# Performance work log

Hardware: AMD Instinct MI355X
Metric: run time of the kernel (lower is better)

The kernel has to match this reference:

```python
import jax, jax.numpy as jnp
import numpy as np

INPUT_DIM = 512
HIDDEN_DIM = 512


def _linear_params(key, in_dim, out_dim):
    kw, kb = jax.random.split(key)
    bound = 1.0 / np.sqrt(in_dim)
    W = jax.random.uniform(kw, (out_dim, in_dim), minval=-bound, maxval=bound, dtype=jnp.float32)
    b = jax.random.uniform(kb, (out_dim,), minval=-bound, maxval=bound, dtype=jnp.float32)
    return W, b


def setup_inputs() -> dict:
    key = jax.random.key(0)
    keys = jax.random.split(key, 11)
    B = 8192
    inp = {
        "x_t": jax.random.normal(keys[0], (B, INPUT_DIM), dtype=jnp.float32),
        "h_tm1": jax.random.normal(keys[1], (B, HIDDEN_DIM), dtype=jnp.float32),
        "c_tm1": jax.random.normal(keys[2], (B, HIDDEN_DIM), dtype=jnp.float32),
    }
    names = ["f_x", "f_h", "i_x", "i_h", "g_x", "g_h", "o_x", "o_h"]
    for n, k in zip(names, keys[3:]):
        in_dim = INPUT_DIM if n.endswith("_x") else HIDDEN_DIM
        W, b = _linear_params(k, in_dim, HIDDEN_DIM)
        inp[f"W_{n}"] = W
        inp[f"b_{n}"] = b
    return inp


def reference(x_t, h_tm1, c_tm1,
              W_f_x, b_f_x, W_f_h, b_f_h,
              W_i_x, b_i_x, W_i_h, b_i_h,
              W_g_x, b_g_x, W_g_h, b_g_h,
              W_o_x, b_o_x, W_o_h, b_o_h):
    # Stacked weights: [4, H, D] -> einsum over D gives [B, 4, H].
    Wx = jnp.stack([W_f_x, W_g_x, W_i_x, W_o_x])  # [4, H, Din]
    bx = jnp.stack([b_f_x, b_g_x, b_i_x, b_o_x])  # [4, H]
    Wh = jnp.stack([W_f_h, W_g_h, W_i_h, W_o_h])
    bh = jnp.stack([b_f_h, b_g_h, b_i_h, b_o_h])
    pre = (jnp.einsum('bd,ghd->bgh', x_t, Wx) + bx
           + jnp.einsum('bd,ghd->bgh', h_tm1, Wh) + bh)  # [B, 4, H]
    f_t = jax.nn.sigmoid(pre[:, 0])
    g_t = jnp.tanh(pre[:, 1])
    i_t = jax.nn.sigmoid(pre[:, 2])
    o_t = jax.nn.sigmoid(pre[:, 3])
    c_t = f_t * c_tm1 + i_t * g_t
    h_t = o_t * jnp.tanh(c_t)
    return (h_t, c_t)
```

## Files before the change

### kernel.cpp

```cpp
#include <hip/hip_runtime.h>
#include <cstdint>
#include <cstddef>


typedef __attribute__((ext_vector_type(8))) short short8;
typedef __attribute__((ext_vector_type(4))) float floatx4;

#define AS1(p) ((const __attribute__((address_space(1))) void*)(p))
#define AS3(p) ((__attribute__((address_space(3))) void*)(p))

__device__ __forceinline__ unsigned short f2bf(float f) {
  union { float f; unsigned u; } v; v.f = f;
  unsigned u = v.u;
  return (unsigned short)((u + 0x7fffu + ((u >> 16) & 1u)) >> 16);
}

__global__ void pack_a_kernel(const float* __restrict__ x,
                              const float* __restrict__ h,
                              unsigned short* __restrict__ A) {
  int e4 = blockIdx.x * 256 + threadIdx.x;
  int e = e4 * 4;
  int b = e >> 10;
  int k = e & 1023;
  const float* src = (k < 512) ? (x + b * 512 + k) : (h + b * 512 + (k - 512));
  float4 v = *(const float4*)src;
  ushort4 o;
  o.x = f2bf(v.x); o.y = f2bf(v.y); o.z = f2bf(v.z); o.w = f2bf(v.w);
  *(ushort4*)(A + e) = o;
}

struct WPtrs {
  const float* wx[4]; const float* wh[4];
  const float* bx[4]; const float* bh[4];
};

__global__ void pack_w_kernel(WPtrs P, unsigned short* __restrict__ B,
                              float* __restrict__ bias) {
  int e4 = blockIdx.x * 256 + threadIdx.x;
  int e = e4 * 4;
  int n = e >> 10;
  int k = e & 1023;
  int g = n >> 9, hh = n & 511;
  const float* src = (k < 512) ? (P.wx[g] + hh * 512 + k)
                               : (P.wh[g] + hh * 512 + (k - 512));
  float4 v = *(const float4*)src;
  ushort4 o;
  o.x = f2bf(v.x); o.y = f2bf(v.y); o.z = f2bf(v.z); o.w = f2bf(v.w);
  *(ushort4*)(B + e) = o;
  if (k == 0) bias[n] = P.bx[g][hh] + P.bh[g][hh];
}

__global__ __launch_bounds__(256)
void lstm_gemm_kernel(const unsigned short* __restrict__ A,
                      const unsigned short* __restrict__ B,
                      const float* __restrict__ bias,
                      const float* __restrict__ c_prev,
                      float* __restrict__ h_out,
                      float* __restrict__ c_out) {
  __shared__ __align__(16) char smem[33792];
  __shared__ float biasS[128];

  const int tid  = threadIdx.x;
  const int lane = tid & 63;
  const int w    = tid >> 6;
  const int quad = lane >> 4;
  const int colA = lane & 15;
  const int m0   = blockIdx.x * 128;
  const int h0   = blockIdx.y * 32;

  if (tid < 128) {
    int g = tid >> 5, hh = tid & 31;
    biasS[tid] = bias[g * 512 + h0 + hh];
  }

  const int srow = tid >> 3;
  const int cl   = tid & 7;
  const int cg   = cl ^ (srow & 7);

  floatx4 acc[4][4];
#pragma unroll
  for (int i = 0; i < 4; ++i)
#pragma unroll
    for (int j = 0; j < 4; ++j) acc[i][j] = (floatx4){0.f, 0.f, 0.f, 0.f};

  const int wm = (w >> 1) * 64;
  const int wn = (w & 1) * 64;

  const char* Ag = (const char*)A;
  const char* Bg = (const char*)B;

  for (int kt = 0; kt < 16; ++kt) {
    __syncthreads();
    const int kb = kt * 128;
#pragma unroll
    for (int j = 0; j < 4; ++j) {
      int r = j * 32 + srow;
      __builtin_amdgcn_global_load_lds(
          AS1(Ag + (size_t)(m0 + r) * 2048 + kb + cg * 16),
          AS3(smem + r * 128 + cl * 16), 16, 0, 0);
      __builtin_amdgcn_global_load_lds(
          AS1(Bg + (size_t)(j * 512 + h0 + srow) * 2048 + kb + cg * 16),
          AS3(smem + 16384 + r * 128 + cl * 16), 16, 0, 0);
    }
    __syncthreads();

#pragma unroll
    for (int kk = 0; kk < 2; ++kk) {
      const int off = ((kk * 4 + quad) ^ (lane & 7)) * 16;
      short8 af[4], bfr[4];
#pragma unroll
      for (int mi = 0; mi < 4; ++mi)
        af[mi] = *(const short8*)(smem + (wm + mi * 16 + colA) * 128 + off);
#pragma unroll
      for (int ni = 0; ni < 4; ++ni)
        bfr[ni] = *(const short8*)(smem + 16384 + (wn + ni * 16 + colA) * 128 + off);
#pragma unroll
      for (int mi = 0; mi < 4; ++mi)
#pragma unroll
        for (int ni = 0; ni < 4; ++ni)
          acc[mi][ni] = __builtin_amdgcn_mfma_f32_16x16x32_bf16(
              af[mi], bfr[ni], acc[mi][ni], 0, 0, 0);
    }
  }

  __syncthreads();
  float* ep = (float*)smem;
#pragma unroll
  for (int rd = 0; rd < 2; ++rd) {
    if ((w >> 1) == rd) {
#pragma unroll
      for (int mi = 0; mi < 4; ++mi)
#pragma unroll
        for (int ni = 0; ni < 4; ++ni) {
          int rr0 = mi * 16 + quad * 4;
          int cc  = wn + ni * 16 + colA;
#pragma unroll
          for (int rr = 0; rr < 4; ++rr)
            ep[(rr0 + rr) * 132 + cc] = acc[mi][ni][rr];
        }
    }
    __syncthreads();
#pragma unroll
    for (int j = 0; j < 8; ++j) {
      int idx  = j * 256 + tid;
      int mloc = idx >> 5;
      int hh   = idx & 31;
      float pf = ep[mloc * 132 +      hh] + biasS[hh];
      float pi = ep[mloc * 132 + 32 + hh] + biasS[32 + hh];
      float pg = ep[mloc * 132 + 64 + hh] + biasS[64 + hh];
      float po = ep[mloc * 132 + 96 + hh] + biasS[96 + hh];
      float fg = 1.f / (1.f + __expf(-pf));
      float ig = 1.f / (1.f + __expf(-pi));
      float gg = 1.f - 2.f / (1.f + __expf(2.f * pg));
      float og = 1.f / (1.f + __expf(-po));
      int m  = m0 + rd * 64 + mloc;
      int hg = h0 + hh;
      float cp = c_prev[m * 512 + hg];
      float cv = fg * cp + ig * gg;
      float th = 1.f - 2.f / (1.f + __expf(2.f * cv));
      h_out[m * 512 + hg] = og * th;
      c_out[m * 512 + hg] = cv;
    }
    __syncthreads();
  }
}

extern "C" void kernel_launch(void* const* d_in, const int* in_sizes, int n_in,
                              void* d_out, int out_size, void* d_ws, size_t ws_size,
                              hipStream_t stream) {
  const float* x = (const float*)d_in[0];
  const float* h = (const float*)d_in[1];
  const float* c = (const float*)d_in[2];

  char* ws = (char*)d_ws;
  unsigned short* Abf = (unsigned short*)ws;
  unsigned short* Bbf = (unsigned short*)(ws + (size_t)16777216);
  float* bias = (float*)(ws + (size_t)16777216 + 4194304);

  float* hout = (float*)d_out;
  float* cout = hout + (size_t)8192 * 512;

  pack_a_kernel<<<8192, 256, 0, stream>>>(x, h, Abf);

  WPtrs P;
  P.wx[0] = (const float*)d_in[3];  P.bx[0] = (const float*)d_in[4];
  P.wh[0] = (const float*)d_in[5];  P.bh[0] = (const float*)d_in[6];
  P.wx[1] = (const float*)d_in[7];  P.bx[1] = (const float*)d_in[8];
  P.wh[1] = (const float*)d_in[9];  P.bh[1] = (const float*)d_in[10];
  P.wx[2] = (const float*)d_in[11]; P.bx[2] = (const float*)d_in[12];
  P.wh[2] = (const float*)d_in[13]; P.bh[2] = (const float*)d_in[14];
  P.wx[3] = (const float*)d_in[15]; P.bx[3] = (const float*)d_in[16];
  P.wh[3] = (const float*)d_in[17]; P.bh[3] = (const float*)d_in[18];
  pack_w_kernel<<<2048, 256, 0, stream>>>(P, Bbf, bias);

  dim3 grid(64, 16);
  lstm_gemm_kernel<<<grid, 256, 0, stream>>>(Abf, Bbf, bias, c, hout, cout);
}
```

Baseline: 179.0 us.

## Merge pack kernels into one launch and use 512-thread GEMM blocks

Folds the activation and weight packing kernels into a single launch that picks its role from the block index, saving one kernel launch. The GEMM block now runs 8 waves of 256 threads instead of 4. Each wave owns a 32x64 sub-tile rather than 64x64, which halves the per-thread accumulator registers. Launch bounds ask for 6 waves per SIMD to raise occupancy and latency hiding. The trade-off is less MFMA work per LDS fragment load per wave, and the bias buffer moves into the main shared array.

```diff
diff --git a/kernel.cpp b/kernel.cpp
--- a/kernel.cpp
+++ b/kernel.cpp
@@ -15,50 +15,47 @@
   return (unsigned short)((u + 0x7fffu + ((u >> 16) & 1u)) >> 16);
 }
 
-__global__ void pack_a_kernel(const float* __restrict__ x,
-                              const float* __restrict__ h,
-                              unsigned short* __restrict__ A) {
-  int e4 = blockIdx.x * 256 + threadIdx.x;
-  int e = e4 * 4;
-  int b = e >> 10;
-  int k = e & 1023;
-  const float* src = (k < 512) ? (x + b * 512 + k) : (h + b * 512 + (k - 512));
-  float4 v = *(const float4*)src;
-  ushort4 o;
-  o.x = f2bf(v.x); o.y = f2bf(v.y); o.z = f2bf(v.z); o.w = f2bf(v.w);
-  *(ushort4*)(A + e) = o;
+struct PackArgs {
+  const float* x; const float* h;
+  const float* wx[4]; const float* wh[4];
+  const float* bx[4]; const float* bh[4];
+  unsigned short* A; unsigned short* B; float* bias;
+};
+
+__global__ __launch_bounds__(256) void pack_all_kernel(PackArgs P) {
+  const int bid = blockIdx.x;
+  if (bid < 8192) {
+    int e = (bid * 256 + threadIdx.x) * 4;
+    int b = e >> 10, k = e & 1023;
+    const float* src = (k < 512) ? (P.x + b * 512 + k)
+                                 : (P.h + b * 512 + (k - 512));
+    float4 v = *(const float4*)src;
+    ushort4 o;
+    o.x = f2bf(v.x); o.y = f2bf(v.y); o.z = f2bf(v.z); o.w = f2bf(v.w);
+    *(ushort4*)(P.A + e) = o;
+  } else {
+    int e = ((bid - 8192) * 256 + threadIdx.x) * 4;
+    int n = e >> 10, k = e & 1023;
+    int g = n >> 9, hh = n & 511;
+    const float* src = (k < 512) ? (P.wx[g] + hh * 512 + k)
+                                 : (P.wh[g] + hh * 512 + (k - 512));
+    float4 v = *(const float4*)src;
+    ushort4 o;
+    o.x = f2bf(v.x); o.y = f2bf(v.y); o.z = f2bf(v.z); o.w = f2bf(v.w);
+    *(ushort4*)(P.B + e) = o;
+    if (k == 0) P.bias[n] = P.bx[g][hh] + P.bh[g][hh];
+  }
 }
 
-struct WPtrs {
-  const float* wx[4]; const float* wh[4];
-  const float* bx[4]; const float* bh[4];
-};
-
-__global__ void pack_w_kernel(WPtrs P, unsigned short* __restrict__ B,
-                              float* __restrict__ bias) {
-  int e4 = blockIdx.x * 256 + threadIdx.x;
-  int e = e4 * 4;
-  int n = e >> 10;
-  int k = e & 1023;
-  int g = n >> 9, hh = n & 511;
-  const float* src = (k < 512) ? (P.wx[g] + hh * 512 + k)
-                               : (P.wh[g] + hh * 512 + (k - 512));
-  float4 v = *(const float4*)src;
-  ushort4 o;
-  o.x = f2bf(v.x); o.y = f2bf(v.y); o.z = f2bf(v.z); o.w = f2bf(v.w);
-  *(ushort4*)(B + e) = o;
-  if (k == 0) bias[n] = P.bx[g][hh] + P.bh[g][hh];
-}
-
-__global__ __launch_bounds__(256)
+__global__ __launch_bounds__(512, 6)
 void lstm_gemm_kernel(const unsigned short* __restrict__ A,
                       const unsigned short* __restrict__ B,
                       const float* __restrict__ bias,
                       const float* __restrict__ c_prev,
                       float* __restrict__ h_out,
                       float* __restrict__ c_out) {
-  __shared__ __align__(16) char smem[33792];
-  __shared__ float biasS[128];
+  __shared__ __align__(16) char smem[34304];
+  float* biasS = (float*)(smem + 33792);
 
   const int tid  = threadIdx.x;
   const int lane = tid & 63;
@@ -77,13 +74,13 @@
   const int cl   = tid & 7;
   const int cg   = cl ^ (srow & 7);
 
-  floatx4 acc[4][4];
+  floatx4 acc[2][4];
 #pragma unroll
-  for (int i = 0; i < 4; ++i)
+  for (int i = 0; i < 2; ++i)
 #pragma unroll
     for (int j = 0; j < 4; ++j) acc[i][j] = (floatx4){0.f, 0.f, 0.f, 0.f};
 
-  const int wm = (w >> 1) * 64;
+  const int wm = (w >> 1) * 32;
   const int wn = (w & 1) * 64;
 
   const char* Ag = (const char*)A;
@@ -93,13 +90,14 @@
     __syncthreads();
     const int kb = kt * 128;
 #pragma unroll
-    for (int j = 0; j < 4; ++j) {
-      int r = j * 32 + srow;
+    for (int j = 0; j < 2; ++j) {
+      int r = j * 64 + srow;
       __builtin_amdgcn_global_load_lds(
           AS1(Ag + (size_t)(m0 + r) * 2048 + kb + cg * 16),
           AS3(smem + r * 128 + cl * 16), 16, 0, 0);
+      int grow = (r >> 5) * 512 + h0 + (r & 31);
       __builtin_amdgcn_global_load_lds(
-          AS1(Bg + (size_t)(j * 512 + h0 + srow) * 2048 + kb + cg * 16),
+          AS1(Bg + (size_t)grow * 2048 + kb + cg * 16),
           AS3(smem + 16384 + r * 128 + cl * 16), 16, 0, 0);
     }
     __syncthreads();
@@ -107,15 +105,15 @@
 #pragma unroll
     for (int kk = 0; kk < 2; ++kk) {
       const int off = ((kk * 4 + quad) ^ (lane & 7)) * 16;
-      short8 af[4], bfr[4];
+      short8 af[2], bfr[4];
 #pragma unroll
-      for (int mi = 0; mi < 4; ++mi)
+      for (int mi = 0; mi < 2; ++mi)
         af[mi] = *(const short8*)(smem + (wm + mi * 16 + colA) * 128 + off);
 #pragma unroll
       for (int ni = 0; ni < 4; ++ni)
         bfr[ni] = *(const short8*)(smem + 16384 + (wn + ni * 16 + colA) * 128 + off);
 #pragma unroll
-      for (int mi = 0; mi < 4; ++mi)
+      for (int mi = 0; mi < 2; ++mi)
 #pragma unroll
         for (int ni = 0; ni < 4; ++ni)
           acc[mi][ni] = __builtin_amdgcn_mfma_f32_16x16x32_bf16(
@@ -127,12 +125,12 @@
   float* ep = (float*)smem;
 #pragma unroll
   for (int rd = 0; rd < 2; ++rd) {
-    if ((w >> 1) == rd) {
+    if ((w >> 2) == rd) {
 #pragma unroll
-      for (int mi = 0; mi < 4; ++mi)
+      for (int mi = 0; mi < 2; ++mi)
 #pragma unroll
         for (int ni = 0; ni < 4; ++ni) {
-          int rr0 = mi * 16 + quad * 4;
+          int rr0 = (wm - rd * 64) + mi * 16 + quad * 4;
           int cc  = wn + ni * 16 + colA;
 #pragma unroll
           for (int rr = 0; rr < 4; ++rr)
@@ -141,8 +139,8 @@
     }
     __syncthreads();
 #pragma unroll
-    for (int j = 0; j < 8; ++j) {
-      int idx  = j * 256 + tid;
+    for (int j = 0; j < 4; ++j) {
+      int idx  = j * 512 + tid;
       int mloc = idx >> 5;
       int hh   = idx & 31;
       float pf = ep[mloc * 132 +      hh] + biasS[hh];
@@ -168,10 +166,6 @@
 extern "C" void kernel_launch(void* const* d_in, const int* in_sizes, int n_in,
                               void* d_out, int out_size, void* d_ws, size_t ws_size,
                               hipStream_t stream) {
-  const float* x = (const float*)d_in[0];
-  const float* h = (const float*)d_in[1];
-  const float* c = (const float*)d_in[2];
-
   char* ws = (char*)d_ws;
   unsigned short* Abf = (unsigned short*)ws;
   unsigned short* Bbf = (unsigned short*)(ws + (size_t)16777216);
@@ -180,9 +174,9 @@
   float* hout = (float*)d_out;
   float* cout = hout + (size_t)8192 * 512;
 
-  pack_a_kernel<<<8192, 256, 0, stream>>>(x, h, Abf);
-
-  WPtrs P;
+  PackArgs P;
+  P.x = (const float*)d_in[0];
+  P.h = (const float*)d_in[1];
   P.wx[0] = (const float*)d_in[3];  P.bx[0] = (const float*)d_in[4];
   P.wh[0] = (const float*)d_in[5];  P.bh[0] = (const float*)d_in[6];
   P.wx[1] = (const float*)d_in[7];  P.bx[1] = (const float*)d_in[8];
@@ -191,8 +185,11 @@
   P.wh[2] = (const float*)d_in[13]; P.bh[2] = (const float*)d_in[14];
   P.wx[3] = (const float*)d_in[15]; P.bx[3] = (const float*)d_in[16];
   P.wh[3] = (const float*)d_in[17]; P.bh[3] = (const float*)d_in[18];
-  pack_w_kernel<<<2048, 256, 0, stream>>>(P, Bbf, bias);
+  P.A = Abf; P.B = Bbf; P.bias = bias;
 
+  pack_all_kernel<<<10240, 256, 0, stream>>>(P);
+
+  const float* c = (const float*)d_in[2];
   dim3 grid(64, 16);
-  lstm_gemm_kernel<<<grid, 256, 0, stream>>>(Abf, Bbf, bias, c, hout, cout);
+  lstm_gemm_kernel<<<grid, 512, 0, stream>>>(Abf, Bbf, bias, c, hout, cout);
 }
```

After: 173.5 us. 3.1% less time.
